# Optimization experiments

Hardware: AMD Instinct MI355X
Metric: run time of the kernel (lower is better)

Reference implementation:

```python
import jax, jax.numpy as jnp
import numpy as np

B, S, C = 8, 1024, 768
H = 12            # num_heads
HD = C // H       # head_dim = 64
QH = QW = 32      # input_size; QH*QW == S


def setup_inputs() -> dict:
    key = jax.random.key(0)
    ks = jax.random.split(key, 6)
    return {
        "x": jax.random.normal(ks[0], (B, S, C), dtype=jnp.float32),
        "w_qkv": jax.random.normal(ks[1], (3 * C, C), dtype=jnp.float32) * 0.02,
        "w_out": jax.random.normal(ks[2], (C, C), dtype=jnp.float32) * 0.02,
        "b_out": jax.random.normal(ks[3], (C,), dtype=jnp.float32) * 0.02,
        "rel_pos_h": jax.random.normal(ks[4], (2 * QH - 1, HD), dtype=jnp.float32) * 0.02,
        "rel_pos_w": jax.random.normal(ks[5], (2 * QW - 1, HD), dtype=jnp.float32) * 0.02,
    }


def reference(x, w_qkv, w_out, b_out, rel_pos_h, rel_pos_w):
    scale = HD ** -0.5
    # qkv projection (no bias), rearrange 'b s (qkv h d) -> qkv b h s d'
    qkv = (x @ w_qkv.T).reshape(B, S, 3, H, HD).transpose(2, 0, 3, 1, 4)
    q, k, v = qkv[0], qkv[1], qkv[2]            # each (B, H, S, HD)

    attn = jnp.einsum('bhxd,bhyd->bhxy', q, k) * scale  # (B, H, S, S)

    # decomposed relative position bias (q_size == k_size, no interpolation)
    idx = jnp.arange(QH)[:, None] - jnp.arange(QH)[None, :] + (QH - 1)
    Rh = rel_pos_h[idx]                          # (QH, QH, HD)
    Rw = rel_pos_w[idx]                          # (QW, QW, HD)
    rq = q.reshape(B * H, QH, QW, HD)
    rel_h = jnp.einsum('bhwc,hkc->bhwk', rq, Rh)  # (BH, QH, QW, QH)
    rel_w = jnp.einsum('bhwc,wkc->bhwk', rq, Rw)  # (BH, QH, QW, QW)
    attn = (attn.reshape(B * H, QH, QW, QH, QW)
            + rel_h[:, :, :, :, None]
            + rel_w[:, :, :, None, :]).reshape(B, H, S, S)

    attn = jax.nn.softmax(attn, axis=-1)
    out = jnp.einsum('bhxy,bhyd->bhxd', attn, v)  # (B, H, S, HD)
    out = out.transpose(0, 2, 1, 3).reshape(B, S, C)
    return out @ w_out.T + b_out
```

## Files before the change

### kernel.cpp

```cpp
#include <hip/hip_runtime.h>
#include <cstdint>
#include <math.h>


using u16 = unsigned short;
using bf16x8 = __attribute__((ext_vector_type(8))) short;
using f32x4  = __attribute__((ext_vector_type(4))) float;

#define LOG2E 1.44269504088896340736f

__device__ __forceinline__ float bf2f(u16 u) {
  union { uint32_t i; float f; } v; v.i = ((uint32_t)u) << 16; return v.f;
}
__device__ __forceinline__ u16 f2bf(float f) {
  union { float f; uint32_t i; } v; v.f = f;
  uint32_t r = v.i + 0x7FFFu + ((v.i >> 16) & 1u);
  return (u16)(r >> 16);
}
__device__ __forceinline__ uint32_t cvt2(float a, float b) {
#if __has_builtin(__builtin_amdgcn_cvt_pk_bf16_f32)
  return __builtin_bit_cast(uint32_t, __builtin_amdgcn_cvt_pk_bf16_f32(a, b));
#else
  return (uint32_t)f2bf(a) | ((uint32_t)f2bf(b) << 16);
#endif
}
__device__ __forceinline__ float fexp2(float x) {
#if __has_builtin(__builtin_amdgcn_exp2f)
  return __builtin_amdgcn_exp2f(x);
#else
  return exp2f(x);
#endif
}
__device__ __forceinline__ uint4 pack8(float4 a, float4 b) {
  uint4 r;
  r.x = cvt2(a.x, a.y); r.y = cvt2(a.z, a.w);
  r.z = cvt2(b.x, b.y); r.w = cvt2(b.z, b.w);
  return r;
}
union U4BF8 { uint4 u; bf16x8 v; };

__device__ __forceinline__ void load16_to_lds(const void* g, void* l) {
  auto gp = reinterpret_cast<const __attribute__((address_space(1))) uint32_t*>(
      reinterpret_cast<uintptr_t>(g));
  auto lp = reinterpret_cast<__attribute__((address_space(3))) uint32_t*>(
      reinterpret_cast<uintptr_t>(l));
  __builtin_amdgcn_global_load_lds(gp, lp, 16, 0, 0);
}

__global__ __launch_bounds__(256, 8)
void cvt_bf16(const float* __restrict__ s0, u16* __restrict__ d0)
{
  int i = (blockIdx.x*256 + threadIdx.x) * 8;
  float4 a = *(const float4*)(s0 + i);
  float4 b = *(const float4*)(s0 + i + 4);
  *(uint4*)(d0 + i) = pack8(a, b);
}

__global__ __launch_bounds__(256, 8)
void cvt_wfrag(const float* __restrict__ wqkv, const float* __restrict__ wout,
               u16* __restrict__ WQF, u16* __restrict__ WOF)
{
  int t = blockIdx.x*256 + threadIdx.x;
  int lane = t & 63;
  int f = t >> 6;
  int nf = f & 7;
  int kstep = (f >> 3) % 24;
  int panel = f / 192;
  int l16 = lane & 15, quad = lane >> 4;
  int k = kstep*32 + quad*8;
  const float* src; u16* dst; int pl, n;
  if (panel < 18) { src = wqkv; dst = WQF; pl = panel; }
  else            { src = wout; dst = WOF; pl = panel - 18; }
  n = pl*128 + nf*16 + l16;
  const float* p = src + (size_t)n*768 + k;
  float4 a = *(const float4*)p;
  float4 b = *(const float4*)(p + 4);
  size_t off = ((size_t)pl*192 + kstep*8 + nf)*512 + (size_t)lane*8;
  *(uint4*)(dst + off) = pack8(a, b);
}

#define GSTEP_ISSUE(KK, BNXT)                                                \
  {                                                                          \
    const int k0_ = ((KK) + 2)*32;                                           \
    __builtin_amdgcn_sched_barrier(0);                                       \
    _Pragma("unroll")                                                        \
    for (int nt = 0; nt < 4; ++nt)                                           \
      BNXT[nt] = *(const bf16x8*)(gB + ((size_t)((KK) + 2)*8 + nt)*512);     \
    char* dA_ = (char*)&sA[((KK) + 2) & 3][0];                               \
    _Pragma("unroll")                                                        \
    for (int it = 0; it < 2; ++it)                                           \
      load16_to_lds(gA[it] + k0_, dA_ + (it*256 + tid)*16);                  \
    __builtin_amdgcn_sched_barrier(0);                                       \
    asm volatile("s_waitcnt vmcnt(12)" ::: "memory");                        \
  }

#define GSTEP_COMPUTE(KK, BCUR)                                              \
  {                                                                          \
    __builtin_amdgcn_s_barrier();                                            \
    __builtin_amdgcn_sched_barrier(0);                                       \
    const u16* sAc_ = &sA[(KK) & 3][0];                                      \
    bf16x8 af_[4];                                                           \
    _Pragma("unroll")                                                        \
    for (int mt = 0; mt < 4; ++mt) {                                         \
      int m = wm*64 + mt*16 + l16;                                           \
      af_[mt] = *(const bf16x8*)&sAc_[(m*4 + (quad ^ ((m >> 1) & 3)))*8];    \
    }                                                                        \
    __builtin_amdgcn_s_setprio(1);                                           \
    _Pragma("unroll")                                                        \
    for (int mt = 0; mt < 4; ++mt)                                           \
      _Pragma("unroll")                                                      \
      for (int nt = 0; nt < 4; ++nt)                                         \
        acc[mt][nt] = __builtin_amdgcn_mfma_f32_16x16x32_bf16(af_[mt], BCUR[nt], acc[mt][nt], 0, 0, 0); \
    __builtin_amdgcn_s_setprio(0);                                           \
    __builtin_amdgcn_sched_barrier(0);                                       \
  }

__global__ __launch_bounds__(256, 3)
void qkv_gemm(const u16* __restrict__ xb, const u16* __restrict__ wqf,
              u16* __restrict__ Q, u16* __restrict__ K, u16* __restrict__ VT)
{
  __shared__ u16 sA[4][128*32];
  const int tid  = threadIdx.x;
  const int lane = tid & 63, wid = tid >> 6;
  const int quad = lane >> 4, l16 = lane & 15;
  const int blk = blockIdx.x;
  const int tn = (blk >> 3) % 18;
  const int tm = (blk & 7) + (blk / 144) * 8;
  const int wm = wid & 1, wn = wid >> 1;

  const u16* gA[2];
  #pragma unroll
  for (int it = 0; it < 2; ++it) {
    int g = it*256 + tid;
    int row = g >> 2;
    int cg  = (g & 3) ^ ((row >> 1) & 3);
    gA[it] = xb + (size_t)(tm*128 + row)*768 + cg*8;
  }
  const u16* gB = wqf + ((size_t)tn*192 + wn*4)*512 + (size_t)lane*8;

  const f32x4 fz = {0.f, 0.f, 0.f, 0.f};
  f32x4 acc[4][4];
  #pragma unroll
  for (int i = 0; i < 4; ++i)
    #pragma unroll
    for (int j = 0; j < 4; ++j) acc[i][j] = fz;

  bf16x8 b0[4], b1[4], b2[4];
  #pragma unroll
  for (int nt = 0; nt < 4; ++nt)
    b0[nt] = *(const bf16x8*)(gB + (size_t)nt*512);
  #pragma unroll
  for (int it = 0; it < 2; ++it)
    load16_to_lds(gA[it], (char*)&sA[0][0] + (it*256 + tid)*16);
  __builtin_amdgcn_sched_barrier(0);
  #pragma unroll
  for (int nt = 0; nt < 4; ++nt)
    b1[nt] = *(const bf16x8*)(gB + (size_t)(8 + nt)*512);
  #pragma unroll
  for (int it = 0; it < 2; ++it)
    load16_to_lds(gA[it] + 32, (char*)&sA[1][0] + (it*256 + tid)*16);
  __builtin_amdgcn_sched_barrier(0);

  for (int i = 0; i < 7; ++i) {
    const int k = i*3;
    GSTEP_ISSUE(k + 0, b2) GSTEP_COMPUTE(k + 0, b0)
    GSTEP_ISSUE(k + 1, b0) GSTEP_COMPUTE(k + 1, b1)
    GSTEP_ISSUE(k + 2, b1) GSTEP_COMPUTE(k + 2, b2)
  }
  GSTEP_ISSUE(21, b2) GSTEP_COMPUTE(21, b0)
  asm volatile("s_waitcnt vmcnt(6)" ::: "memory");
  GSTEP_COMPUTE(22, b1)
  asm volatile("s_waitcnt vmcnt(0)" ::: "memory");
  GSTEP_COMPUTE(23, b2)

  const float KSCL = 0.125f * LOG2E;
  #pragma unroll
  for (int mt = 0; mt < 4; ++mt) {
    #pragma unroll
    for (int nt = 0; nt < 4; ++nt) {
      const int col = wn*64 + nt*16 + l16;
      const int n = tn*128 + col;
      #pragma unroll
      for (int r = 0; r < 4; ++r) {
        const int rowin = wm*64 + mt*16 + quad*4 + r;
        const int m = tm*128 + rowin;
        const int b = m >> 10, s = m & 1023;
        if (n < 768) {
          int h = n >> 6, d = n & 63;
          Q[(((size_t)b*12 + h)*1024 + s)*64 + d] = f2bf(acc[mt][nt][r]);
        } else if (n < 1536) {
          int nn = n - 768; int h = nn >> 6, d = nn & 63;
          int bh = b*12 + h;
          int kb = s >> 7, srel = s & 127;
          K[(size_t)bh*65536
            + (((kb*8 + (srel >> 4))*2 + (d >> 5))*4 + ((d >> 3) & 3))*128
            + (srel & 15)*8 + (d & 7)] = f2bf(acc[mt][nt][r] * KSCL);
        } else {
          int nn = n - 1536; int h = nn >> 6, d = nn & 63;
          int bh = b*12 + h;
          int kb = s >> 7, srel = s & 127;
          VT[(size_t)bh*65536
             + ((((kb*2 + (srel >> 6))*2 + ((srel >> 5) & 1))*4 + (d >> 4))*4 + ((srel >> 3) & 3))*128
             + (d & 15)*8 + (srel & 7)] = f2bf(acc[mt][nt][r]);
        }
      }
    }
  }
}

__global__ __launch_bounds__(256, 4)
void rel_bias(const u16* __restrict__ Q, const float* __restrict__ rph, const float* __restrict__ rpw,
              u16* __restrict__ RH, u16* __restrict__ RW)
{
  const int tid  = threadIdx.x;
  const int lane = tid & 63, wid = tid >> 6;
  const int quad = lane >> 4, l16 = lane & 15;
  const int blk = blockIdx.x;
  const int gx = (blk >> 3) & 7;
  const int bh = (blk & 7) + (blk >> 6) * 8;
  const bool isW = gx >= 4;
  const float* rp = isW ? rpw : rph;
  u16* RO = isW ? RW : RH;
  const int qb = (gx & 3)*8 + wid*2;
  const f32x4 fz = {0.f, 0.f, 0.f, 0.f};

  #pragma unroll
  for (int gi = 0; gi < 2; ++gi) {
    const int qv = qb + gi;
    f32x4 acc[2][2];
    #pragma unroll
    for (int i = 0; i < 2; ++i)
      #pragma unroll
      for (int j = 0; j < 2; ++j) acc[i][j] = fz;

    #pragma unroll
    for (int ks = 0; ks < 2; ++ks) {
      bf16x8 af[2], bfv[2];
      #pragma unroll
      for (int mt = 0; mt < 2; ++mt) {
        int m = mt*16 + l16;
        int xrow = isW ? (m*32 + qv) : (qv*32 + m);
        af[mt] = *(const bf16x8*)(Q + ((size_t)bh*1024 + xrow)*64 + ks*32 + quad*8);
      }
      #pragma unroll
      for (int nt = 0; nt < 2; ++nt) {
        int n = nt*16 + l16;
        const float* bp = rp + (size_t)(qv - n + 31)*64 + ks*32 + quad*8;
        U4BF8 c; c.u = pack8(*(const float4*)bp, *(const float4*)(bp + 4));
        bfv[nt] = c.v;
      }
      #pragma unroll
      for (int mt = 0; mt < 2; ++mt)
        #pragma unroll
        for (int nt = 0; nt < 2; ++nt)
          acc[mt][nt] = __builtin_amdgcn_mfma_f32_16x16x32_bf16(af[mt], bfv[nt], acc[mt][nt], 0, 0, 0);
    }
    #pragma unroll
    for (int mt = 0; mt < 2; ++mt)
      #pragma unroll
      for (int nt = 0; nt < 2; ++nt)
        #pragma unroll
        for (int r = 0; r < 4; ++r) {
          int j = mt*16 + quad*4 + r;
          int xrow = isW ? (j*32 + qv) : (qv*32 + j);
          int n = nt*16 + l16;
          RO[((size_t)bh*1024 + xrow)*32 + n] = f2bf(acc[mt][nt][r] * LOG2E);
        }
  }
}

__global__ __launch_bounds__(512, 4)
void attn_kernel(const u16* __restrict__ Q, const u16* __restrict__ KF, const u16* __restrict__ VF,
                 const u16* __restrict__ RH, const u16* __restrict__ RW, u16* __restrict__ AO)
{
  __shared__ u16 sK[2][8192];
  __shared__ u16 sV[2][8192];
  __shared__ u16 sP[128*64];
  const int tid  = threadIdx.x;
  const int lane = tid & 63, wid = tid >> 6;
  const int quad = lane >> 4, l16 = lane & 15;
  const int blk = blockIdx.x;
  const int qt = (blk >> 3) & 7;
  const int bh = (blk & 7) + (blk >> 6) * 8;
  const int q0 = qt * 128;
  const int ql = wid*16 + l16;

  bf16x8 qf[2];
  #pragma unroll
  for (int ks = 0; ks < 2; ++ks)
    qf[ks] = *(const bf16x8*)(Q + ((size_t)bh*1024 + q0 + ql)*64 + ks*32 + quad*8);

  const size_t ro = ((size_t)bh*1024 + q0 + ql)*32;
  float bwv[2][4];
  #pragma unroll
  for (int h2 = 0; h2 < 2; ++h2) {
    uint2 t = *(const uint2*)(RW + ro + h2*16 + quad*4);
    bwv[h2][0] = bf2f((u16)(t.x & 0xFFFF));
    bwv[h2][1] = bf2f((u16)(t.x >> 16));
    bwv[h2][2] = bf2f((u16)(t.y & 0xFFFF));
    bwv[h2][3] = bf2f((u16)(t.y >> 16));
  }

  const u16* KFs = KF + (size_t)bh*65536;
  const u16* VFs = VF + (size_t)bh*65536;

  load16_to_lds(KFs + tid*8,        (char*)&sK[0][0] + tid*16);
  load16_to_lds(KFs + 4096 + tid*8, (char*)&sK[0][0] + 8192 + tid*16);
  load16_to_lds(VFs + tid*8,        (char*)&sV[0][0] + tid*16);
  load16_to_lds(VFs + 4096 + tid*8, (char*)&sV[0][0] + 8192 + tid*16);

  const f32x4 fz = {0.f, 0.f, 0.f, 0.f};
  f32x4 lsv = fz;
  f32x4 accO[4];
  #pragma unroll
  for (int dt = 0; dt < 4; ++dt) accO[dt] = fz;

  int cur = 0;
  for (int kb = 0; kb < 8; ++kb) {
    uint2 bhl = *(const uint2*)(RH + ro + kb*4);

    if (kb < 7) {
      const u16* ks = KFs + (size_t)(kb + 1)*8192;
      const u16* vs = VFs + (size_t)(kb + 1)*8192;
      char* dk = (char*)&sK[cur ^ 1][0];
      char* dv = (char*)&sV[cur ^ 1][0];
      __builtin_amdgcn_sched_barrier(0);
      load16_to_lds(ks + tid*8,        dk + tid*16);
      load16_to_lds(ks + 4096 + tid*8, dk + 8192 + tid*16);
      load16_to_lds(vs + tid*8,        dv + tid*16);
      load16_to_lds(vs + 4096 + tid*8, dv + 8192 + tid*16);
      __builtin_amdgcn_sched_barrier(0);
      asm volatile("s_waitcnt vmcnt(4)" ::: "memory");
    } else {
      asm volatile("s_waitcnt vmcnt(0)" ::: "memory");
    }
    __builtin_amdgcn_s_barrier();
    __builtin_amdgcn_sched_barrier(0);

    const u16* sKc = &sK[cur][0];
    const u16* sVc = &sV[cur][0];

    #pragma unroll
    for (int h = 0; h < 2; ++h) {
      f32x4 sAcc[4];
      #pragma unroll
      for (int smt = 0; smt < 4; ++smt) {
        const int g = h*2 + (smt >> 1);
        const uint32_t gw = (g < 2) ? bhl.x : bhl.y;
        const float bhf = bf2f((u16)(gw >> ((g & 1)*16)));
        #pragma unroll
        for (int r = 0; r < 4; ++r) sAcc[smt][r] = bhf + bwv[smt & 1][r];
      }
      __builtin_amdgcn_s_setprio(1);
      #pragma unroll
      for (int ks = 0; ks < 2; ++ks) {
        #pragma unroll
        for (int smt = 0; smt < 4; ++smt) {
          bf16x8 af = *(const bf16x8*)&sKc[(size_t)(((h*4 + smt)*2 + ks))*512 + lane*8];
          sAcc[smt] = __builtin_amdgcn_mfma_f32_16x16x32_bf16(af, qf[ks], sAcc[smt], 0, 0, 0);
        }
      }
      __builtin_amdgcn_s_setprio(0);

      #pragma unroll
      for (int smt = 0; smt < 4; ++smt) {
        #pragma unroll
        for (int r = 0; r < 4; ++r) {
          float p = fexp2(sAcc[smt][r]);
          sAcc[smt][r] = p;
          lsv[r] += p;
        }
      }

      #pragma unroll
      for (int smt = 0; smt < 4; ++smt) {
        uint2 w;
        w.x = cvt2(sAcc[smt][0], sAcc[smt][1]);
        w.y = cvt2(sAcc[smt][2], sAcc[smt][3]);
        const int sg = smt*2 + (quad >> 1);
        *(uint2*)&sP[ql*64 + ((sg ^ (ql & 7))*8) + (quad & 1)*4] = w;
      }

      #pragma unroll
      for (int ka = 0; ka < 2; ++ka) {
        bf16x8 pf = *(const bf16x8*)&sP[ql*64 + (((ka*4 + quad) ^ (ql & 7))*8)];
        __builtin_amdgcn_s_setprio(1);
        #pragma unroll
        for (int dt = 0; dt < 4; ++dt) {
          bf16x8 vf = *(const bf16x8*)&sVc[(size_t)(((h*2 + ka)*4 + dt))*512 + lane*8];
          accO[dt] = __builtin_amdgcn_mfma_f32_16x16x32_bf16(vf, pf, accO[dt], 0, 0, 0);
        }
        __builtin_amdgcn_s_setprio(0);
      }
    }

    __builtin_amdgcn_sched_barrier(0);
    __builtin_amdgcn_s_barrier();
    __builtin_amdgcn_sched_barrier(0);
    cur ^= 1;
  }

  const int b = bh / 12, head = bh % 12;
  float s = lsv[0] + lsv[1] + lsv[2] + lsv[3];
  s += __shfl_xor(s, 16);
  s += __shfl_xor(s, 32);
  const float inv = 1.f / s;
  const size_t base = ((size_t)(b*1024 + q0 + ql))*768 + head*64;
  #pragma unroll
  for (int dt = 0; dt < 4; ++dt) {
    uint2 o;
    o.x = cvt2(accO[dt][0]*inv, accO[dt][1]*inv);
    o.y = cvt2(accO[dt][2]*inv, accO[dt][3]*inv);
    *(uint2*)&AO[base + dt*16 + quad*4] = o;
  }
}

__global__ __launch_bounds__(256, 3)
void out_gemm(const u16* __restrict__ A, const u16* __restrict__ wof, const float* __restrict__ bout,
              float* __restrict__ out)
{
  __shared__ u16 sA[4][128*32];
  const int tid  = threadIdx.x;
  const int lane = tid & 63, wid = tid >> 6;
  const int quad = lane >> 4, l16 = lane & 15;
  const int blk = blockIdx.x;
  const int tn = (blk >> 3) % 6;
  const int tm = (blk & 7) + (blk / 48) * 8;
  const int wm = wid & 1, wn = wid >> 1;

  const u16* gA[2];
  #pragma unroll
  for (int it = 0; it < 2; ++it) {
    int g = it*256 + tid;
    int row = g >> 2;
    int cg  = (g & 3) ^ ((row >> 1) & 3);
    gA[it] = A + (size_t)(tm*128 + row)*768 + cg*8;
  }
  const u16* gB = wof + ((size_t)tn*192 + wn*4)*512 + (size_t)lane*8;

  const f32x4 fz = {0.f, 0.f, 0.f, 0.f};
  f32x4 acc[4][4];
  #pragma unroll
  for (int i = 0; i < 4; ++i)
    #pragma unroll
    for (int j = 0; j < 4; ++j) acc[i][j] = fz;

  bf16x8 b0[4], b1[4], b2[4];
  #pragma unroll
  for (int nt = 0; nt < 4; ++nt)
    b0[nt] = *(const bf16x8*)(gB + (size_t)nt*512);
  #pragma unroll
  for (int it = 0; it < 2; ++it)
    load16_to_lds(gA[it], (char*)&sA[0][0] + (it*256 + tid)*16);
  __builtin_amdgcn_sched_barrier(0);
  #pragma unroll
  for (int nt = 0; nt < 4; ++nt)
    b1[nt] = *(const bf16x8*)(gB + (size_t)(8 + nt)*512);
  #pragma unroll
  for (int it = 0; it < 2; ++it)
    load16_to_lds(gA[it] + 32, (char*)&sA[1][0] + (it*256 + tid)*16);
  __builtin_amdgcn_sched_barrier(0);

  for (int i = 0; i < 7; ++i) {
    const int k = i*3;
    GSTEP_ISSUE(k + 0, b2) GSTEP_COMPUTE(k + 0, b0)
    GSTEP_ISSUE(k + 1, b0) GSTEP_COMPUTE(k + 1, b1)
    GSTEP_ISSUE(k + 2, b1) GSTEP_COMPUTE(k + 2, b2)
  }
  GSTEP_ISSUE(21, b2) GSTEP_COMPUTE(21, b0)
  asm volatile("s_waitcnt vmcnt(6)" ::: "memory");
  GSTEP_COMPUTE(22, b1)
  asm volatile("s_waitcnt vmcnt(0)" ::: "memory");
  GSTEP_COMPUTE(23, b2)

  #pragma unroll
  for (int mt = 0; mt < 4; ++mt) {
    #pragma unroll
    for (int nt = 0; nt < 4; ++nt) {
      const int n = tn*128 + wn*64 + nt*16 + l16;
      const float bv = bout[n];
      #pragma unroll
      for (int r = 0; r < 4; ++r) {
        const int rowin = wm*64 + mt*16 + quad*4 + r;
        out[(size_t)(tm*128 + rowin)*768 + n] = acc[mt][nt][r] + bv;
      }
    }
  }
}

extern "C" void kernel_launch(void* const* d_in, const int* in_sizes, int n_in,
                              void* d_out, int out_size, void* d_ws, size_t ws_size,
                              hipStream_t stream)
{
  const float* x    = (const float*)d_in[0];
  const float* wqkv = (const float*)d_in[1];
  const float* wout = (const float*)d_in[2];
  const float* bout = (const float*)d_in[3];
  const float* rph  = (const float*)d_in[4];
  const float* rpw  = (const float*)d_in[5];
  float* out = (float*)d_out;

  char* ws = (char*)d_ws;
  const size_t SZ = (size_t)96*1024*64;
  u16* Q   = (u16*)ws;
  u16* K   = Q  + SZ;
  u16* VT  = K  + SZ;
  u16* RH  = VT + SZ;
  u16* RW  = RH + (size_t)96*1024*32;
  u16* AO  = RW + (size_t)96*1024*32;
  u16* xb  = AO + SZ;
  u16* wqf = xb + SZ;
  u16* wof = wqf + (size_t)2304*768;

  cvt_bf16   <<<dim3(3072), dim3(256), 0, stream>>>(x, xb);
  cvt_wfrag  <<<dim3(1152), dim3(256), 0, stream>>>(wqkv, wout, wqf, wof);
  qkv_gemm   <<<dim3(1152), dim3(256), 0, stream>>>(xb, wqf, Q, K, VT);
  rel_bias   <<<dim3(768),  dim3(256), 0, stream>>>(Q, rph, rpw, RH, RW);
  attn_kernel<<<dim3(768),  dim3(512), 0, stream>>>(Q, K, VT, RH, RW, AO);
  out_gemm   <<<dim3(384),  dim3(256), 0, stream>>>(AO, wof, bout, out);
}
```

Measured before the change: 206.0 us.

## Merge conversion kernels and deepen GEMM K-step to 64 with triple-buffered LDS

Fuses the two fp32-to-bf16 conversion kernels into a single launch to save one kernel launch. Restructures both the QKV and output GEMMs to process 64-wide K steps (two MFMA k-substeps) per barrier, using a 3-stage LDS ring of 128x64 tiles with an 8-way XOR swizzle and double-buffered B-fragment registers. This halves the number of barriers and pipeline steps, at the cost of more in-flight registers for B fragments and a shallower prefetch distance (one step ahead instead of two).

```diff
diff --git a/kernel.cpp b/kernel.cpp
--- a/kernel.cpp
+++ b/kernel.cpp
@@ -48,70 +48,75 @@
 }
 
 __global__ __launch_bounds__(256, 8)
-void cvt_bf16(const float* __restrict__ s0, u16* __restrict__ d0)
-{
-  int i = (blockIdx.x*256 + threadIdx.x) * 8;
-  float4 a = *(const float4*)(s0 + i);
-  float4 b = *(const float4*)(s0 + i + 4);
-  *(uint4*)(d0 + i) = pack8(a, b);
-}
-
-__global__ __launch_bounds__(256, 8)
-void cvt_wfrag(const float* __restrict__ wqkv, const float* __restrict__ wout,
-               u16* __restrict__ WQF, u16* __restrict__ WOF)
-{
-  int t = blockIdx.x*256 + threadIdx.x;
-  int lane = t & 63;
-  int f = t >> 6;
-  int nf = f & 7;
-  int kstep = (f >> 3) % 24;
-  int panel = f / 192;
-  int l16 = lane & 15, quad = lane >> 4;
-  int k = kstep*32 + quad*8;
-  const float* src; u16* dst; int pl, n;
-  if (panel < 18) { src = wqkv; dst = WQF; pl = panel; }
-  else            { src = wout; dst = WOF; pl = panel - 18; }
-  n = pl*128 + nf*16 + l16;
-  const float* p = src + (size_t)n*768 + k;
-  float4 a = *(const float4*)p;
-  float4 b = *(const float4*)(p + 4);
-  size_t off = ((size_t)pl*192 + kstep*8 + nf)*512 + (size_t)lane*8;
-  *(uint4*)(dst + off) = pack8(a, b);
-}
-
-#define GSTEP_ISSUE(KK, BNXT)                                                \
+void cvt_all(const float* __restrict__ x, const float* __restrict__ wqkv,
+             const float* __restrict__ wout, u16* __restrict__ xb,
+             u16* __restrict__ WQF, u16* __restrict__ WOF)
+{
+  const int blk = blockIdx.x;
+  if (blk < 3072) {
+    int i = (blk*256 + threadIdx.x) * 8;
+    float4 a = *(const float4*)(x + i);
+    float4 b = *(const float4*)(x + i + 4);
+    *(uint4*)(xb + i) = pack8(a, b);
+  } else {
+    int t = (blk - 3072)*256 + threadIdx.x;
+    int lane = t & 63;
+    int f = t >> 6;
+    int nf = f & 7;
+    int kstep = (f >> 3) % 24;
+    int panel = f / 192;
+    int l16 = lane & 15, quad = lane >> 4;
+    int k = kstep*32 + quad*8;
+    const float* src; u16* dst; int pl, n;
+    if (panel < 18) { src = wqkv; dst = WQF; pl = panel; }
+    else            { src = wout; dst = WOF; pl = panel - 18; }
+    n = pl*128 + nf*16 + l16;
+    const float* p = src + (size_t)n*768 + k;
+    float4 a = *(const float4*)p;
+    float4 b = *(const float4*)(p + 4);
+    size_t off = ((size_t)pl*192 + kstep*8 + nf)*512 + (size_t)lane*8;
+    *(uint4*)(dst + off) = pack8(a, b);
+  }
+}
+
+#define QSTEP_ISSUE(KK, BN)                                                  \
   {                                                                          \
-    const int k0_ = ((KK) + 2)*32;                                           \
+    const int kn_ = (KK) + 1;                                                \
     __builtin_amdgcn_sched_barrier(0);                                       \
     _Pragma("unroll")                                                        \
-    for (int nt = 0; nt < 4; ++nt)                                           \
-      BNXT[nt] = *(const bf16x8*)(gB + ((size_t)((KK) + 2)*8 + nt)*512);     \
-    char* dA_ = (char*)&sA[((KK) + 2) & 3][0];                               \
+    for (int ks = 0; ks < 2; ++ks)                                           \
+      _Pragma("unroll")                                                      \
+      for (int nt = 0; nt < 4; ++nt)                                         \
+        BN[ks][nt] = *(const bf16x8*)(gB + ((size_t)(kn_*2 + ks)*8 + nt)*512); \
+    char* dA_ = (char*)&sA[kn_ % 3][0];                                      \
     _Pragma("unroll")                                                        \
-    for (int it = 0; it < 2; ++it)                                           \
-      load16_to_lds(gA[it] + k0_, dA_ + (it*256 + tid)*16);                  \
+    for (int it = 0; it < 4; ++it)                                           \
+      load16_to_lds(gA0 + (size_t)it*(32*768) + kn_*64, dA_ + (it*256 + tid)*16); \
     __builtin_amdgcn_sched_barrier(0);                                       \
     asm volatile("s_waitcnt vmcnt(12)" ::: "memory");                        \
   }
 
-#define GSTEP_COMPUTE(KK, BCUR)                                              \
+#define QSTEP_COMPUTE(KK, BC)                                                \
   {                                                                          \
     __builtin_amdgcn_s_barrier();                                            \
     __builtin_amdgcn_sched_barrier(0);                                       \
-    const u16* sAc_ = &sA[(KK) & 3][0];                                      \
-    bf16x8 af_[4];                                                           \
+    const u16* sAc_ = &sA[(KK) % 3][0];                                      \
     _Pragma("unroll")                                                        \
-    for (int mt = 0; mt < 4; ++mt) {                                         \
-      int m = wm*64 + mt*16 + l16;                                           \
-      af_[mt] = *(const bf16x8*)&sAc_[(m*4 + (quad ^ ((m >> 1) & 3)))*8];    \
+    for (int ks = 0; ks < 2; ++ks) {                                         \
+      bf16x8 af_[4];                                                         \
+      _Pragma("unroll")                                                      \
+      for (int mt = 0; mt < 4; ++mt) {                                       \
+        int m = wm*64 + mt*16 + l16;                                         \
+        af_[mt] = *(const bf16x8*)&sAc_[(m*8 + ((ks*4 + quad) ^ (m & 7)))*8]; \
+      }                                                                      \
+      __builtin_amdgcn_s_setprio(1);                                         \
+      _Pragma("unroll")                                                      \
+      for (int mt = 0; mt < 4; ++mt)                                         \
+        _Pragma("unroll")                                                    \
+        for (int nt = 0; nt < 4; ++nt)                                       \
+          acc[mt][nt] = __builtin_amdgcn_mfma_f32_16x16x32_bf16(af_[mt], BC[ks][nt], acc[mt][nt], 0, 0, 0); \
+      __builtin_amdgcn_s_setprio(0);                                         \
     }                                                                        \
-    __builtin_amdgcn_s_setprio(1);                                           \
-    _Pragma("unroll")                                                        \
-    for (int mt = 0; mt < 4; ++mt)                                           \
-      _Pragma("unroll")                                                      \
-      for (int nt = 0; nt < 4; ++nt)                                         \
-        acc[mt][nt] = __builtin_amdgcn_mfma_f32_16x16x32_bf16(af_[mt], BCUR[nt], acc[mt][nt], 0, 0, 0); \
-    __builtin_amdgcn_s_setprio(0);                                           \
     __builtin_amdgcn_sched_barrier(0);                                       \
   }
 
@@ -119,7 +124,7 @@
 void qkv_gemm(const u16* __restrict__ xb, const u16* __restrict__ wqf,
               u16* __restrict__ Q, u16* __restrict__ K, u16* __restrict__ VT)
 {
-  __shared__ u16 sA[4][128*32];
+  __shared__ u16 sA[3][128*64];
   const int tid  = threadIdx.x;
   const int lane = tid & 63, wid = tid >> 6;
   const int quad = lane >> 4, l16 = lane & 15;
@@ -128,14 +133,9 @@
   const int tm = (blk & 7) + (blk / 144) * 8;
   const int wm = wid & 1, wn = wid >> 1;
 
-  const u16* gA[2];
-  #pragma unroll
-  for (int it = 0; it < 2; ++it) {
-    int g = it*256 + tid;
-    int row = g >> 2;
-    int cg  = (g & 3) ^ ((row >> 1) & 3);
-    gA[it] = xb + (size_t)(tm*128 + row)*768 + cg*8;
-  }
+  const int row0 = tid >> 3;
+  const int cg0  = (tid & 7) ^ (row0 & 7);
+  const u16* gA0 = xb + (size_t)(tm*128 + row0)*768 + cg0*8;
   const u16* gB = wqf + ((size_t)tn*192 + wn*4)*512 + (size_t)lane*8;
 
   const f32x4 fz = {0.f, 0.f, 0.f, 0.f};
@@ -145,33 +145,25 @@
     #pragma unroll
     for (int j = 0; j < 4; ++j) acc[i][j] = fz;
 
-  bf16x8 b0[4], b1[4], b2[4];
-  #pragma unroll
-  for (int nt = 0; nt < 4; ++nt)
-    b0[nt] = *(const bf16x8*)(gB + (size_t)nt*512);
-  #pragma unroll
-  for (int it = 0; it < 2; ++it)
-    load16_to_lds(gA[it], (char*)&sA[0][0] + (it*256 + tid)*16);
+  bf16x8 b0[2][4], b1[2][4];
+  #pragma unroll
+  for (int ks = 0; ks < 2; ++ks)
+    #pragma unroll
+    for (int nt = 0; nt < 4; ++nt)
+      b0[ks][nt] = *(const bf16x8*)(gB + ((size_t)ks*8 + nt)*512);
+  #pragma unroll
+  for (int it = 0; it < 4; ++it)
+    load16_to_lds(gA0 + (size_t)it*(32*768), (char*)&sA[0][0] + (it*256 + tid)*16);
   __builtin_amdgcn_sched_barrier(0);
-  #pragma unroll
-  for (int nt = 0; nt < 4; ++nt)
-    b1[nt] = *(const bf16x8*)(gB + (size_t)(8 + nt)*512);
-  #pragma unroll
-  for (int it = 0; it < 2; ++it)
-    load16_to_lds(gA[it] + 32, (char*)&sA[1][0] + (it*256 + tid)*16);
-  __builtin_amdgcn_sched_barrier(0);
-
-  for (int i = 0; i < 7; ++i) {
-    const int k = i*3;
-    GSTEP_ISSUE(k + 0, b2) GSTEP_COMPUTE(k + 0, b0)
-    GSTEP_ISSUE(k + 1, b0) GSTEP_COMPUTE(k + 1, b1)
-    GSTEP_ISSUE(k + 2, b1) GSTEP_COMPUTE(k + 2, b2)
-  }
-  GSTEP_ISSUE(21, b2) GSTEP_COMPUTE(21, b0)
-  asm volatile("s_waitcnt vmcnt(6)" ::: "memory");
-  GSTEP_COMPUTE(22, b1)
+
+  for (int i = 0; i < 5; ++i) {
+    const int k = i*2;
+    QSTEP_ISSUE(k + 0, b1) QSTEP_COMPUTE(k + 0, b0)
+    QSTEP_ISSUE(k + 1, b0) QSTEP_COMPUTE(k + 1, b1)
+  }
+  QSTEP_ISSUE(10, b1) QSTEP_COMPUTE(10, b0)
   asm volatile("s_waitcnt vmcnt(0)" ::: "memory");
-  GSTEP_COMPUTE(23, b2)
+  QSTEP_COMPUTE(11, b1)
 
   const float KSCL = 0.125f * LOG2E;
   #pragma unroll
@@ -419,7 +411,7 @@
 void out_gemm(const u16* __restrict__ A, const u16* __restrict__ wof, const float* __restrict__ bout,
               float* __restrict__ out)
 {
-  __shared__ u16 sA[4][128*32];
+  __shared__ u16 sA[3][128*64];
   const int tid  = threadIdx.x;
   const int lane = tid & 63, wid = tid >> 6;
   const int quad = lane >> 4, l16 = lane & 15;
@@ -428,14 +420,9 @@
   const int tm = (blk & 7) + (blk / 48) * 8;
   const int wm = wid & 1, wn = wid >> 1;
 
-  const u16* gA[2];
-  #pragma unroll
-  for (int it = 0; it < 2; ++it) {
-    int g = it*256 + tid;
-    int row = g >> 2;
-    int cg  = (g & 3) ^ ((row >> 1) & 3);
-    gA[it] = A + (size_t)(tm*128 + row)*768 + cg*8;
-  }
+  const int row0 = tid >> 3;
+  const int cg0  = (tid & 7) ^ (row0 & 7);
+  const u16* gA0 = A + (size_t)(tm*128 + row0)*768 + cg0*8;
   const u16* gB = wof + ((size_t)tn*192 + wn*4)*512 + (size_t)lane*8;
 
   const f32x4 fz = {0.f, 0.f, 0.f, 0.f};
@@ -445,33 +432,25 @@
     #pragma unroll
     for (int j = 0; j < 4; ++j) acc[i][j] = fz;
 
-  bf16x8 b0[4], b1[4], b2[4];
-  #pragma unroll
-  for (int nt = 0; nt < 4; ++nt)
-    b0[nt] = *(const bf16x8*)(gB + (size_t)nt*512);
-  #pragma unroll
-  for (int it = 0; it < 2; ++it)
-    load16_to_lds(gA[it], (char*)&sA[0][0] + (it*256 + tid)*16);
+  bf16x8 b0[2][4], b1[2][4];
+  #pragma unroll
+  for (int ks = 0; ks < 2; ++ks)
+    #pragma unroll
+    for (int nt = 0; nt < 4; ++nt)
+      b0[ks][nt] = *(const bf16x8*)(gB + ((size_t)ks*8 + nt)*512);
+  #pragma unroll
+  for (int it = 0; it < 4; ++it)
+    load16_to_lds(gA0 + (size_t)it*(32*768), (char*)&sA[0][0] + (it*256 + tid)*16);
   __builtin_amdgcn_sched_barrier(0);
-  #pragma unroll
-  for (int nt = 0; nt < 4; ++nt)
-    b1[nt] = *(const bf16x8*)(gB + (size_t)(8 + nt)*512);
-  #pragma unroll
-  for (int it = 0; it < 2; ++it)
-    load16_to_lds(gA[it] + 32, (char*)&sA[1][0] + (it*256 + tid)*16);
-  __builtin_amdgcn_sched_barrier(0);
-
-  for (int i = 0; i < 7; ++i) {
-    const int k = i*3;
-    GSTEP_ISSUE(k + 0, b2) GSTEP_COMPUTE(k + 0, b0)
-    GSTEP_ISSUE(k + 1, b0) GSTEP_COMPUTE(k + 1, b1)
-    GSTEP_ISSUE(k + 2, b1) GSTEP_COMPUTE(k + 2, b2)
-  }
-  GSTEP_ISSUE(21, b2) GSTEP_COMPUTE(21, b0)
-  asm volatile("s_waitcnt vmcnt(6)" ::: "memory");
-  GSTEP_COMPUTE(22, b1)
+
+  for (int i = 0; i < 5; ++i) {
+    const int k = i*2;
+    QSTEP_ISSUE(k + 0, b1) QSTEP_COMPUTE(k + 0, b0)
+    QSTEP_ISSUE(k + 1, b0) QSTEP_COMPUTE(k + 1, b1)
+  }
+  QSTEP_ISSUE(10, b1) QSTEP_COMPUTE(10, b0)
   asm volatile("s_waitcnt vmcnt(0)" ::: "memory");
-  GSTEP_COMPUTE(23, b2)
+  QSTEP_COMPUTE(11, b1)
 
   #pragma unroll
   for (int mt = 0; mt < 4; ++mt) {
@@ -512,8 +491,7 @@
   u16* wqf = xb + SZ;
   u16* wof = wqf + (size_t)2304*768;
 
-  cvt_bf16   <<<dim3(3072), dim3(256), 0, stream>>>(x, xb);
-  cvt_wfrag  <<<dim3(1152), dim3(256), 0, stream>>>(wqkv, wout, wqf, wof);
+  cvt_all    <<<dim3(4224), dim3(256), 0, stream>>>(x, wqkv, wout, xb, wqf, wof);
   qkv_gemm   <<<dim3(1152), dim3(256), 0, stream>>>(xb, wqf, Q, K, VT);
   rel_bias   <<<dim3(768),  dim3(256), 0, stream>>>(Q, rph, rpw, RH, RW);
   attn_kernel<<<dim3(768),  dim3(512), 0, stream>>>(Q, K, VT, RH, RW, AO);
```

New measurement: 202.9 us. About the same (-1.5%).
